# Kernel tuning notes

Measured on AMD Instinct MI355X. Metric: run time of the kernel, lower is better.

## Reference

```python
import jax, jax.numpy as jnp
import numpy as np

DEPTH = 30
IN_C, OUT_C, WIDTH = 1, 1, 1
DILATIONS = [i + 1 for i in range(10)]


def setup_inputs() -> dict:
    key = jax.random.key(0)
    ks = jax.random.split(key, 9)
    B, H, W = 4, 512, 512
    # MSDConvBlock weight init std from the source
    std = float(np.sqrt(2.0 / (9.0 * (IN_C + WIDTH * (DEPTH - 1)) + OUT_C)))
    x = jax.random.normal(ks[0], (B, IN_C, H, W), dtype=jnp.float32)
    # Wmsd[i, :i+1] are the 3x3 kernels at depth i: channel 0 acts on x,
    # channel z acts on hiddenstate z-1. Padded rows are unused.
    Wmsd = jax.random.normal(ks[1], (DEPTH, DEPTH, 3, 3), dtype=jnp.float32) * std
    bias = jax.random.normal(ks[2], (DEPTH,), dtype=jnp.float32) * 0.1  # shared per-depth bias
    # final 1x1 conv (zero-init in source; random here so the output is non-trivial)
    convW = jax.random.normal(ks[3], (OUT_C, WIDTH * DEPTH + IN_C, 1, 1), dtype=jnp.float32) * 0.1
    convB = jax.random.normal(ks[4], (OUT_C,), dtype=jnp.float32) * 0.1
    # ScalingBlocks: per-channel affine, identity init
    sin_w = jnp.ones((IN_C,), dtype=jnp.float32)
    sin_b = jnp.zeros((IN_C,), dtype=jnp.float32)
    sout_w = jnp.ones((OUT_C,), dtype=jnp.float32)
    sout_b = jnp.zeros((OUT_C,), dtype=jnp.float32)
    return {"x": x, "Wmsd": Wmsd, "bias": bias, "convW": convW, "convB": convB,
            "sin_w": sin_w, "sin_b": sin_b, "sout_w": sout_w, "sout_b": sout_b}


def _conv(x, w, dilation):
    # 'same' 3x3 dilated conv, NCHW / OIHW
    d = dilation
    return jax.lax.conv_general_dilated(
        x, w, window_strides=(1, 1), padding=[(d, d), (d, d)],
        rhs_dilation=(d, d), dimension_numbers=("NCHW", "OIHW", "NCHW"))


def reference(x, Wmsd, bias, convW, convB, sin_w, sin_b, sout_w, sout_b):
    depth = Wmsd.shape[0]
    x = x * sin_w[None, :, None, None] + sin_b[None, :, None, None]
    feats = x  # growing concat: [x, h0, h1, ...]
    for i in range(depth):
        d = DILATIONS[i % len(DILATIONS)]  # counter increments once per depth
        n_in = feats.shape[1]  # = IN_C + i (with width=1, IN_C=1)
        w = Wmsd[i, :n_in][None]  # [1, n_in, 3, 3]
        # sum of single-channel convs == one multi-channel conv over the concat
        h = _conv(feats, w, d)
        h = jax.nn.relu(h + bias[i])
        feats = jnp.concatenate([feats, h], axis=1)
    y = jax.lax.conv_general_dilated(
        feats, convW, window_strides=(1, 1), padding="VALID",
        dimension_numbers=("NCHW", "OIHW", "NCHW"))
    y = y + convB[None, :, None, None]
    y = y * sout_w[None, :, None, None] + sout_b[None, :, None, None]
    return y
```

## Files before the change

kernel.cpp:

```cpp
#include <hip/hip_runtime.h>


#define MSD_DEPTH 30
#define NB 4
#define IH 512
#define IW 512
#define HALO 16
#define WPp (IW + 2 * HALO)
#define HPp (IH + 2 * HALO)
#define PLANE_U ((size_t)WPp * HPp)
#define PSTR ((size_t)NB * PLANE_U)
#define NPAIR 15
#define NPIX (NB * IH * IW)
#define WPK_OFF ((size_t)20 << 20)
#define ZSTRIPS (32 * (WPp / 4) * NPAIR * NB)
#define SSTRIPS (512 * 8 * NPAIR * NB)
#define TOTZ (ZSTRIPS + SSTRIPS)

typedef _Float16 h2v __attribute__((ext_vector_type(2)));
typedef unsigned int u32;

__device__ __forceinline__ float fdot2u(u32 a, u32 b, float c) {
#if __has_builtin(__builtin_amdgcn_fdot2)
    return __builtin_amdgcn_fdot2(__builtin_bit_cast(h2v, a),
                                  __builtin_bit_cast(h2v, b), c, false);
#else
    h2v x = __builtin_bit_cast(h2v, a), y = __builtin_bit_cast(h2v, b);
    return c + (float)x[0] * (float)y[0] + (float)x[1] * (float)y[1];
#endif
}

__global__ __launch_bounds__(256) void preamble_kernel(const float* __restrict__ x,
                                                       const float* __restrict__ Wmsd,
                                                       const float* __restrict__ convW,
                                                       u32* __restrict__ feats,
                                                       u32* __restrict__ wpk,
                                                       u32* __restrict__ cpk,
                                                       const float* __restrict__ sw,
                                                       const float* __restrict__ sb) {
    int idx = blockIdx.x * 256 + threadIdx.x;

    if (idx < MSD_DEPTH * NPAIR * 9) {
        int I = idx / (NPAIR * 9);
        int rem = idx - I * (NPAIR * 9);
        int p = rem / 9, t = rem - p * 9;
        int NC = I + 1, c0 = 2 * p, c1 = 2 * p + 1;
        h2v pk;
        pk[0] = (_Float16)((c0 < NC) ? Wmsd[((size_t)I * MSD_DEPTH + c0) * 9 + t] : 0.f);
        pk[1] = (_Float16)((c1 < NC) ? Wmsd[((size_t)I * MSD_DEPTH + c1) * 9 + t] : 0.f);
        wpk[idx] = __builtin_bit_cast(u32, pk);
    }
    if (idx < NPAIR) {
        h2v pk;
        pk[0] = (_Float16)convW[2 * idx];
        pk[1] = (_Float16)convW[2 * idx + 1];
        cpk[idx] = __builtin_bit_cast(u32, pk);
    }

    if (idx < ZSTRIPS) {
        const int per = 32 * (WPp / 4);
        int sub = idx / per;
        int s = idx - sub * per;
        int rr = s / 136;
        int c4 = (s - rr * 136) * 4;
        int r = (rr < 16) ? rr : (IH + HALO) + (rr - 16);
        uint4 z = {0, 0, 0, 0};
        *(uint4*)(feats + (size_t)sub * PLANE_U + (size_t)r * WPp + c4) = z;
    } else if (idx < TOTZ) {
        int s = idx - ZSTRIPS;
        int sub = s >> 12;
        int rem = s & 4095;
        int r = HALO + (rem >> 3);
        int e = rem & 7;
        int c4 = (e < 4) ? (e * 4) : (IW + HALO + (e - 4) * 4);
        uint4 z = {0, 0, 0, 0};
        *(uint4*)(feats + (size_t)sub * PLANE_U + (size_t)r * WPp + c4) = z;
    }

    if (idx < NPIX / 8) {
        int pix = idx * 8;
        int b = pix >> 18;
        int y = (pix >> 9) & 511;
        int xx = pix & 511;
        const float sws = sw[0], sbs = sb[0];
        u32 v[8];
#pragma unroll
        for (int j = 0; j < 8; ++j) {
            _Float16 h = (_Float16)(x[pix + j] * sws + sbs);
            v[j] = (u32)__builtin_bit_cast(unsigned short, h);
        }
        u32* q = feats + (size_t)b * PLANE_U + (size_t)(y + HALO) * WPp + HALO + xx;
        *(uint4*)q = *(uint4*)&v[0];
        *(uint4*)(q + 4) = *(uint4*)&v[4];
    }
}

template <int I, int MINW>
__global__ __launch_bounds__(512, MINW) void depth_kernel(u32* __restrict__ feats,
                                                          const u32* __restrict__ wpk,
                                                          const u32* __restrict__ cpk,
                                                          const float* __restrict__ bias,
                                                          const float* __restrict__ convW,
                                                          const float* __restrict__ convB,
                                                          const float* __restrict__ soutw,
                                                          const float* __restrict__ soutb,
                                                          float* __restrict__ out) {
    constexpr int D = (I % 10) + 1;
    constexpr int NC = I + 1;
    constexpr int NP = (NC + 1) / 2;
    constexpr bool LAST = (I == MSD_DEPTH - 1);
    constexpr int C0 = (12 - D) >> 2;
    constexpr int C1 = (15 + D) >> 2;

    const int tid = threadIdx.x;
    const int widx = tid >> 6, lane = tid & 63;
    const int bid = blockIdx.x;
    const int xcd = bid & 7;
    const int kk = bid >> 3;
    const int b = xcd >> 1;
    const int y = (xcd & 1) * 256 + kk * 4 + (widx >> 1);
    const int h = widx & 1;
    const int xx = h * 256 + lane * 4;

    u32* const pb = feats + (size_t)b * PLANE_U + (size_t)(y + HALO) * WPp + HALO + xx;

    float acc[4], ydot[4];
#pragma unroll
    for (int j = 0; j < 4; ++j) { acc[j] = 0.f; ydot[j] = 0.f; }

    const u32* const wrb = wpk + (size_t)I * (NPAIR * 9);

    u32 A[3][28], B[3][28];

    auto load_pair = [&](u32 (*bp)[28], int p) {
        const u32* pp = pb + (size_t)p * PSTR;
#pragma unroll
        for (int r = 0; r < 3; ++r) {
            const u32* rp = pp + (ptrdiff_t)(r - 1) * (D * WPp);
#pragma unroll
            for (int c = C0; c <= C1; ++c)
                *(uint4*)&bp[r][4 * c] = *(const uint4*)(rp - 12 + 4 * c);
        }
    };

    auto compute = [&](u32 (*bp)[28], int p) {
        const u32* wq = wrb + p * 9;
        const u32 cw = LAST ? cpk[p] : 0u;
#pragma unroll
        for (int r = 0; r < 3; ++r) {
            const u32* s = bp[r];
            const u32 w0 = wq[r * 3 + 0], w1 = wq[r * 3 + 1], w2 = wq[r * 3 + 2];
#pragma unroll
            for (int k = 0; k < 4; ++k) {
                float a = acc[k];
                a = fdot2u(s[12 - D + k], w0, a);
                a = fdot2u(s[12 + k],     w1, a);
                a = fdot2u(s[12 + D + k], w2, a);
                acc[k] = a;
            }
            if (LAST && r == 1) {
#pragma unroll
                for (int k = 0; k < 4; ++k) ydot[k] = fdot2u(s[12 + k], cw, ydot[k]);
            }
        }
    };

    load_pair(A, 0);
    int p = 0;
    for (; p + 2 <= NP; p += 2) {
        load_pair(B, p + 1);
        compute(A, p);
        if (p + 2 < NP) load_pair(A, p + 2);
        compute(B, p + 1);
    }
    if (p < NP) compute(A, p);

    const float b0 = bias[I];
    if (!LAST) {
        u32 part[4];
        if constexpr ((NC & 1) != 0) {
            constexpr bool inA = (((NP - 1) & 1) == 0);
            const u32* s = inA ? A[1] : B[1];
#pragma unroll
            for (int j = 0; j < 4; ++j) part[j] = s[12 + j];
        }
        u32 mg[4];
#pragma unroll
        for (int j = 0; j < 4; ++j) {
            float hh = acc[j] + b0;
            hh = hh > 0.f ? hh : 0.f;
            u32 h16 = (u32)__builtin_bit_cast(unsigned short, (_Float16)hh);
            if constexpr ((NC & 1) != 0)
                mg[j] = (part[j] & 0xFFFFu) | (h16 << 16);
            else
                mg[j] = h16;
        }
        u32* q = feats + (size_t)(NC >> 1) * PSTR + (size_t)b * PLANE_U +
                 (size_t)(y + HALO) * WPp + HALO + xx;
        *(uint4*)q = *(uint4*)&mg[0];
    } else {
        const float cw30 = convW[MSD_DEPTH];
        const float cb = convB[0], ow = soutw[0], ob = soutb[0];
        float* q = out + ((size_t)b * IH + y) * IW + xx;
        float o[4];
#pragma unroll
        for (int j = 0; j < 4; ++j) {
            float hh = acc[j] + b0;
            hh = hh > 0.f ? hh : 0.f;
            float yv = ydot[j] + cw30 * hh + cb;
            o[j] = yv * ow + ob;
        }
        *(uint4*)q = *(uint4*)&o[0];
    }
}

extern "C" void kernel_launch(void* const* d_in, const int* in_sizes, int n_in,
                              void* d_out, int out_size, void* d_ws, size_t ws_size,
                              hipStream_t stream) {
    const float* x     = (const float*)d_in[0];
    const float* Wmsd  = (const float*)d_in[1];
    const float* bias  = (const float*)d_in[2];
    const float* convW = (const float*)d_in[3];
    const float* convB = (const float*)d_in[4];
    const float* sinw  = (const float*)d_in[5];
    const float* sinb  = (const float*)d_in[6];
    const float* soutw = (const float*)d_in[7];
    const float* soutb = (const float*)d_in[8];
    float* out = (float*)d_out;

    u32* feats = (u32*)d_ws;
    u32* wpk = feats + WPK_OFF;
    u32* cpk = wpk + MSD_DEPTH * NPAIR * 9;

    preamble_kernel<<<(TOTZ + 255) / 256, 256, 0, stream>>>(x, Wmsd, convW,
                                                            feats, wpk, cpk,
                                                            sinw, sinb);

#define LNCH(I)                                                                     \
    depth_kernel<I, (((I % 10) + 1 <= 4) ? 4 : 3)><<<512, 512, 0, stream>>>(        \
        feats, wpk, cpk, bias, convW, convB, soutw, soutb, out);
    LNCH(0)  LNCH(1)  LNCH(2)  LNCH(3)  LNCH(4)
    LNCH(5)  LNCH(6)  LNCH(7)  LNCH(8)  LNCH(9)
    LNCH(10) LNCH(11) LNCH(12) LNCH(13) LNCH(14)
    LNCH(15) LNCH(16) LNCH(17) LNCH(18) LNCH(19)
    LNCH(20) LNCH(21) LNCH(22) LNCH(23) LNCH(24)
    LNCH(25) LNCH(26) LNCH(27) LNCH(28) LNCH(29)
#undef LNCH
}
```

Baseline: 382.5 us.

## Fuse all depth layers into one cooperative kernel with per-row dataflow flags

After: 1.471 ms. +284.6%, slower.

```diff
diff --git a/kernel.cpp b/kernel.cpp
--- a/kernel.cpp
+++ b/kernel.cpp
@@ -12,6 +12,8 @@
 #define PSTR ((size_t)NB * PLANE_U)
 #define NPAIR 15
 #define NPIX (NB * IH * IW)
+#define FLAGS_OFF ((size_t)18 << 20)
+#define NFLAGS (MSD_DEPTH * NB * IH)
 #define WPK_OFF ((size_t)20 << 20)
 #define ZSTRIPS (32 * (WPp / 4) * NPAIR * NB)
 #define SSTRIPS (512 * 8 * NPAIR * NB)
@@ -28,6 +30,13 @@
     h2v x = __builtin_bit_cast(h2v, a), y = __builtin_bit_cast(h2v, b);
     return c + (float)x[0] * (float)y[0] + (float)x[1] * (float)y[1];
 #endif
+}
+
+__device__ __forceinline__ u32 aload_sys(const u32* p) {
+    return __hip_atomic_load(p, __ATOMIC_RELAXED, __HIP_MEMORY_SCOPE_SYSTEM);
+}
+__device__ __forceinline__ void astore_sys(u32* p, u32 v) {
+    __hip_atomic_store(p, v, __ATOMIC_RELAXED, __HIP_MEMORY_SCOPE_SYSTEM);
 }
 
 __global__ __launch_bounds__(256) void preamble_kernel(const float* __restrict__ x,
@@ -39,6 +48,8 @@
                                                        const float* __restrict__ sw,
                                                        const float* __restrict__ sb) {
     int idx = blockIdx.x * 256 + threadIdx.x;
+
+    if (idx < NFLAGS) feats[FLAGS_OFF + idx] = 0u;
 
     if (idx < MSD_DEPTH * NPAIR * 9) {
         int I = idx / (NPAIR * 9);
@@ -95,23 +106,181 @@
     }
 }
 
-template <int I, int MINW>
-__global__ __launch_bounds__(512, MINW) void depth_kernel(u32* __restrict__ feats,
-                                                          const u32* __restrict__ wpk,
-                                                          const u32* __restrict__ cpk,
-                                                          const float* __restrict__ bias,
-                                                          const float* __restrict__ convW,
-                                                          const float* __restrict__ convB,
-                                                          const float* __restrict__ soutw,
-                                                          const float* __restrict__ soutb,
-                                                          float* __restrict__ out) {
+template <int I, bool MEGA>
+__device__ __forceinline__ void depth_body(int b, int y, int xx, int lane,
+                                           u32* __restrict__ feats,
+                                           const u32* __restrict__ wpk,
+                                           const u32* __restrict__ cpk,
+                                           const float* __restrict__ bias,
+                                           const float* __restrict__ convW,
+                                           const float* __restrict__ convB,
+                                           const float* __restrict__ soutw,
+                                           const float* __restrict__ soutb,
+                                           float* __restrict__ out,
+                                           u32* __restrict__ flags) {
     constexpr int D = (I % 10) + 1;
     constexpr int NC = I + 1;
     constexpr int NP = (NC + 1) / 2;
     constexpr bool LAST = (I == MSD_DEPTH - 1);
     constexpr int C0 = (12 - D) >> 2;
     constexpr int C1 = (15 + D) >> 2;
-
+    constexpr bool HASAT = MEGA && (I >= 1);
+    constexpr int NPP = HASAT ? NP - 1 : NP;
+
+    if constexpr (HASAT) {
+        if (lane == 0) {
+            u32* fb = flags + ((size_t)(I - 1) * NB + b) * IH;
+#pragma unroll
+            for (int t = 0; t < 3; ++t) {
+                int r = (t == 0) ? (y - D) : (t == 1) ? y : (y + D);
+                if (r < 0 || r >= IH) continue;
+                while (__hip_atomic_load(&fb[r], __ATOMIC_RELAXED,
+                                         __HIP_MEMORY_SCOPE_SYSTEM) < 2u)
+                    __builtin_amdgcn_s_sleep(2);
+            }
+        }
+        asm volatile("" ::: "memory");
+        __builtin_amdgcn_sched_barrier(0);
+    }
+
+    u32* const pb = feats + (size_t)b * PLANE_U + (size_t)(y + HALO) * WPp + HALO + xx;
+
+    float acc[4], ydot[4];
+#pragma unroll
+    for (int j = 0; j < 4; ++j) { acc[j] = 0.f; ydot[j] = 0.f; }
+
+    const u32* const wrb = wpk + (size_t)I * (NPAIR * 9);
+
+    u32 A[3][28], B[3][28];
+
+    auto load_pair = [&](u32 (*bp)[28], int p) {
+        const u32* pp = pb + (size_t)p * PSTR;
+#pragma unroll
+        for (int r = 0; r < 3; ++r) {
+            const u32* rp = pp + (ptrdiff_t)(r - 1) * (D * WPp);
+#pragma unroll
+            for (int c = C0; c <= C1; ++c)
+                *(uint4*)&bp[r][4 * c] = *(const uint4*)(rp - 12 + 4 * c);
+        }
+    };
+
+    auto load_pair_at = [&](u32 (*bp)[28], int p) {
+        const u32* pp = pb + (size_t)p * PSTR;
+#pragma unroll
+        for (int r = 0; r < 3; ++r) {
+            const u32* rp = pp + (ptrdiff_t)(r - 1) * (D * WPp) - 12;
+#pragma unroll
+            for (int c = C0; c <= C1; ++c)
+#pragma unroll
+                for (int j = 0; j < 4; ++j)
+                    bp[r][4 * c + j] = aload_sys(rp + 4 * c + j);
+        }
+    };
+
+    auto compute = [&](u32 (*bp)[28], int p) {
+        const u32* wq = wrb + p * 9;
+        const u32 cw = LAST ? cpk[p] : 0u;
+#pragma unroll
+        for (int r = 0; r < 3; ++r) {
+            const u32* s = bp[r];
+            const u32 w0 = wq[r * 3 + 0], w1 = wq[r * 3 + 1], w2 = wq[r * 3 + 2];
+#pragma unroll
+            for (int k = 0; k < 4; ++k) {
+                float a = acc[k];
+                a = fdot2u(s[12 - D + k], w0, a);
+                a = fdot2u(s[12 + k],     w1, a);
+                a = fdot2u(s[12 + D + k], w2, a);
+                acc[k] = a;
+            }
+            if (LAST && r == 1) {
+#pragma unroll
+                for (int k = 0; k < 4; ++k) ydot[k] = fdot2u(s[12 + k], cw, ydot[k]);
+            }
+        }
+    };
+
+    if constexpr (NPP > 0) {
+        load_pair(A, 0);
+        int p = 0;
+        for (; p + 2 <= NPP; p += 2) {
+            load_pair(B, p + 1);
+            compute(A, p);
+            if (p + 2 < NPP) load_pair(A, p + 2);
+            compute(B, p + 1);
+        }
+        if (p < NPP) compute(A, p);
+    }
+
+    if constexpr (HASAT) {
+        load_pair_at(A, NP - 1);
+        compute(A, NP - 1);
+    }
+
+    const float b0 = bias[I];
+    if (!LAST) {
+        u32 part[4];
+        if constexpr ((NC & 1) != 0) {
+            if constexpr (HASAT) {
+#pragma unroll
+                for (int j = 0; j < 4; ++j) part[j] = A[1][12 + j];
+            } else {
+                constexpr bool inA = (((NP - 1) & 1) == 0);
+                const u32* s = inA ? A[1] : B[1];
+#pragma unroll
+                for (int j = 0; j < 4; ++j) part[j] = s[12 + j];
+            }
+        }
+        u32 mg[4];
+#pragma unroll
+        for (int j = 0; j < 4; ++j) {
+            float hh = acc[j] + b0;
+            hh = hh > 0.f ? hh : 0.f;
+            u32 h16 = (u32)__builtin_bit_cast(unsigned short, (_Float16)hh);
+            if constexpr ((NC & 1) != 0)
+                mg[j] = (part[j] & 0xFFFFu) | (h16 << 16);
+            else
+                mg[j] = h16;
+        }
+        u32* q = feats + (size_t)(NC >> 1) * PSTR + (size_t)b * PLANE_U +
+                 (size_t)(y + HALO) * WPp + HALO + xx;
+        if constexpr (MEGA) {
+            astore_sys(q + 0, mg[0]);
+            astore_sys(q + 1, mg[1]);
+            astore_sys(q + 2, mg[2]);
+            astore_sys(q + 3, mg[3]);
+            asm volatile("s_waitcnt vmcnt(0)" ::: "memory");
+            if (lane == 0)
+                __hip_atomic_fetch_add(flags + ((size_t)I * NB + b) * IH + y, 1u,
+                                       __ATOMIC_RELAXED, __HIP_MEMORY_SCOPE_SYSTEM);
+        } else {
+            *(uint4*)q = *(uint4*)&mg[0];
+        }
+    } else {
+        const float cw30 = convW[MSD_DEPTH];
+        const float cb = convB[0], ow = soutw[0], ob = soutb[0];
+        float* q = out + ((size_t)b * IH + y) * IW + xx;
+        float o[4];
+#pragma unroll
+        for (int j = 0; j < 4; ++j) {
+            float hh = acc[j] + b0;
+            hh = hh > 0.f ? hh : 0.f;
+            float yv = ydot[j] + cw30 * hh + cb;
+            o[j] = yv * ow + ob;
+        }
+        *(uint4*)q = *(uint4*)&o[0];
+    }
+}
+
+template <int I>
+__global__ __launch_bounds__(512, 4) void depth4_kernel(u32* __restrict__ feats,
+                                                        const u32* __restrict__ wpk,
+                                                        const u32* __restrict__ cpk,
+                                                        const float* __restrict__ bias,
+                                                        const float* __restrict__ convW,
+                                                        const float* __restrict__ convB,
+                                                        const float* __restrict__ soutw,
+                                                        const float* __restrict__ soutb,
+                                                        float* __restrict__ out) {
     const int tid = threadIdx.x;
     const int widx = tid >> 6, lane = tid & 63;
     const int bid = blockIdx.x;
@@ -121,97 +290,40 @@
     const int y = (xcd & 1) * 256 + kk * 4 + (widx >> 1);
     const int h = widx & 1;
     const int xx = h * 256 + lane * 4;
-
-    u32* const pb = feats + (size_t)b * PLANE_U + (size_t)(y + HALO) * WPp + HALO + xx;
-
-    float acc[4], ydot[4];
-#pragma unroll
-    for (int j = 0; j < 4; ++j) { acc[j] = 0.f; ydot[j] = 0.f; }
-
-    const u32* const wrb = wpk + (size_t)I * (NPAIR * 9);
-
-    u32 A[3][28], B[3][28];
-
-    auto load_pair = [&](u32 (*bp)[28], int p) {
-        const u32* pp = pb + (size_t)p * PSTR;
-#pragma unroll
-        for (int r = 0; r < 3; ++r) {
-            const u32* rp = pp + (ptrdiff_t)(r - 1) * (D * WPp);
-#pragma unroll
-            for (int c = C0; c <= C1; ++c)
-                *(uint4*)&bp[r][4 * c] = *(const uint4*)(rp - 12 + 4 * c);
-        }
-    };
-
-    auto compute = [&](u32 (*bp)[28], int p) {
-        const u32* wq = wrb + p * 9;
-        const u32 cw = LAST ? cpk[p] : 0u;
-#pragma unroll
-        for (int r = 0; r < 3; ++r) {
-            const u32* s = bp[r];
-            const u32 w0 = wq[r * 3 + 0], w1 = wq[r * 3 + 1], w2 = wq[r * 3 + 2];
-#pragma unroll
-            for (int k = 0; k < 4; ++k) {
-                float a = acc[k];
-                a = fdot2u(s[12 - D + k], w0, a);
-                a = fdot2u(s[12 + k],     w1, a);
-                a = fdot2u(s[12 + D + k], w2, a);
-                acc[k] = a;
-            }
-            if (LAST && r == 1) {
-#pragma unroll
-                for (int k = 0; k < 4; ++k) ydot[k] = fdot2u(s[12 + k], cw, ydot[k]);
-            }
-        }
-    };
-
-    load_pair(A, 0);
-    int p = 0;
-    for (; p + 2 <= NP; p += 2) {
-        load_pair(B, p + 1);
-        compute(A, p);
-        if (p + 2 < NP) load_pair(A, p + 2);
-        compute(B, p + 1);
-    }
-    if (p < NP) compute(A, p);
-
-    const float b0 = bias[I];
-    if (!LAST) {
-        u32 part[4];
-        if constexpr ((NC & 1) != 0) {
-            constexpr bool inA = (((NP - 1) & 1) == 0);
-            const u32* s = inA ? A[1] : B[1];
-#pragma unroll
-            for (int j = 0; j < 4; ++j) part[j] = s[12 + j];
-        }
-        u32 mg[4];
-#pragma unroll
-        for (int j = 0; j < 4; ++j) {
-            float hh = acc[j] + b0;
-            hh = hh > 0.f ? hh : 0.f;
-            u32 h16 = (u32)__builtin_bit_cast(unsigned short, (_Float16)hh);
-            if constexpr ((NC & 1) != 0)
-                mg[j] = (part[j] & 0xFFFFu) | (h16 << 16);
-            else
-                mg[j] = h16;
-        }
-        u32* q = feats + (size_t)(NC >> 1) * PSTR + (size_t)b * PLANE_U +
-                 (size_t)(y + HALO) * WPp + HALO + xx;
-        *(uint4*)q = *(uint4*)&mg[0];
-    } else {
-        const float cw30 = convW[MSD_DEPTH];
-        const float cb = convB[0], ow = soutw[0], ob = soutb[0];
-        float* q = out + ((size_t)b * IH + y) * IW + xx;
-        float o[4];
-#pragma unroll
-        for (int j = 0; j < 4; ++j) {
-            float hh = acc[j] + b0;
-            hh = hh > 0.f ? hh : 0.f;
-            float yv = ydot[j] + cw30 * hh + cb;
-            o[j] = yv * ow + ob;
-        }
-        *(uint4*)q = *(uint4*)&o[0];
-    }
+    depth_body<I, false>(b, y, xx, lane, feats, wpk, cpk, bias, convW, convB,
+                         soutw, soutb, out, nullptr);
+}
+
+__global__ __launch_bounds__(512, 4) void msd_mega(u32* __restrict__ feats,
+                                                   const u32* __restrict__ wpk,
+                                                   const u32* __restrict__ cpk,
+                                                   const float* __restrict__ bias,
+                                                   const float* __restrict__ convW,
+                                                   const float* __restrict__ convB,
+                                                   const float* __restrict__ soutw,
+                                                   const float* __restrict__ soutb,
+                                                   float* __restrict__ out,
+                                                   u32* __restrict__ flags) {
+    const int tid = threadIdx.x;
+    const int widx = tid >> 6, lane = tid & 63;
+    const int bid = blockIdx.x;
+    const int xcd = bid & 7;
+    const int kk = bid >> 3;
+    const int b = xcd >> 1;
+    const int y = (xcd & 1) * 256 + kk * 4 + (widx >> 1);
+    const int h = widx & 1;
+    const int xx = h * 256 + lane * 4;
+
+#define PH(I)                                                                  \
+    depth_body<I, true>(b, y, xx, lane, feats, wpk, cpk, bias, convW, convB,   \
+                        soutw, soutb, out, flags);
+    PH(0)  PH(1)  PH(2)  PH(3)  PH(4)
+    PH(5)  PH(6)  PH(7)  PH(8)  PH(9)
+    PH(10) PH(11) PH(12) PH(13) PH(14)
+    PH(15) PH(16) PH(17) PH(18) PH(19)
+    PH(20) PH(21) PH(22) PH(23) PH(24)
+    PH(25) PH(26) PH(27) PH(28) PH(29)
+#undef PH
 }
 
 extern "C" void kernel_launch(void* const* d_in, const int* in_sizes, int n_in,
@@ -229,6 +341,7 @@
     float* out = (float*)d_out;
 
     u32* feats = (u32*)d_ws;
+    u32* flags = feats + FLAGS_OFF;
     u32* wpk = feats + WPK_OFF;
     u32* cpk = wpk + MSD_DEPTH * NPAIR * 9;
 
@@ -236,14 +349,19 @@
                                                             feats, wpk, cpk,
                                                             sinw, sinb);
 
-#define LNCH(I)                                                                     \
-    depth_kernel<I, (((I % 10) + 1 <= 4) ? 4 : 3)><<<512, 512, 0, stream>>>(        \
-        feats, wpk, cpk, bias, convW, convB, soutw, soutb, out);
-    LNCH(0)  LNCH(1)  LNCH(2)  LNCH(3)  LNCH(4)
-    LNCH(5)  LNCH(6)  LNCH(7)  LNCH(8)  LNCH(9)
-    LNCH(10) LNCH(11) LNCH(12) LNCH(13) LNCH(14)
-    LNCH(15) LNCH(16) LNCH(17) LNCH(18) LNCH(19)
-    LNCH(20) LNCH(21) LNCH(22) LNCH(23) LNCH(24)
-    LNCH(25) LNCH(26) LNCH(27) LNCH(28) LNCH(29)
+    void* args[] = {&feats, &wpk, &cpk, &bias, &convW, &convB,
+                    &soutw, &soutb, &out, &flags};
+    hipError_t rc = hipLaunchCooperativeKernel(msd_mega, dim3(512), dim3(512),
+                                               args, 0u, stream);
+    if (rc != hipSuccess) {
+        (void)hipGetLastError();
+#define LNCH(I) depth4_kernel<I><<<512, 512, 0, stream>>>(feats, wpk, cpk, bias, convW, convB, soutw, soutb, out);
+        LNCH(0)  LNCH(1)  LNCH(2)  LNCH(3)  LNCH(4)
+        LNCH(5)  LNCH(6)  LNCH(7)  LNCH(8)  LNCH(9)
+        LNCH(10) LNCH(11) LNCH(12) LNCH(13) LNCH(14)
+        LNCH(15) LNCH(16) LNCH(17) LNCH(18) LNCH(19)
+        LNCH(20) LNCH(21) LNCH(22) LNCH(23) LNCH(24)
+        LNCH(25) LNCH(26) LNCH(27) LNCH(28) LNCH(29)
 #undef LNCH
-}
+    }
+}
```

## Fuse consecutive depth layers into one kernel with shared-memory halo recompute

Applied to the files above, without the earlier changes.

New measurement: 740.3 us. 1.94x slower.

```diff
diff --git a/kernel.cpp b/kernel.cpp
--- a/kernel.cpp
+++ b/kernel.cpp
@@ -95,122 +95,210 @@
     }
 }
 
-template <int I, int MINW>
-__global__ __launch_bounds__(512, MINW) void depth_kernel(u32* __restrict__ feats,
-                                                          const u32* __restrict__ wpk,
-                                                          const u32* __restrict__ cpk,
-                                                          const float* __restrict__ bias,
-                                                          const float* __restrict__ convW,
-                                                          const float* __restrict__ convB,
-                                                          const float* __restrict__ soutw,
-                                                          const float* __restrict__ soutb,
-                                                          float* __restrict__ out) {
-    constexpr int D = (I % 10) + 1;
-    constexpr int NC = I + 1;
-    constexpr int NP = (NC + 1) / 2;
-    constexpr bool LAST = (I == MSD_DEPTH - 1);
-    constexpr int C0 = (12 - D) >> 2;
-    constexpr int C1 = (15 + D) >> 2;
+template <int I>
+__global__ __launch_bounds__(512, 4) void fused_kernel(u32* __restrict__ feats,
+                                                       const u32* __restrict__ wpk,
+                                                       const u32* __restrict__ cpk,
+                                                       const float* __restrict__ bias,
+                                                       const float* __restrict__ convW,
+                                                       const float* __restrict__ convB,
+                                                       const float* __restrict__ soutw,
+                                                       const float* __restrict__ soutb,
+                                                       float* __restrict__ out) {
+    constexpr int D1 = (I % 10) + 1;
+    constexpr int D2 = ((I + 1) % 10) + 1;
+    constexpr int NP = I / 2 + 1;
+    constexpr bool LAST = (I == MSD_DEPTH - 2);
+    constexpr int HR = 4 + 2 * D2;
+    constexpr int ITER = HR / 4;
+    constexpr int C01 = (12 - D1) >> 2, C11 = (15 + D1) >> 2;
+    constexpr int C02 = (12 - D2) >> 2, C12 = (15 + D2) >> 2;
+    constexpr int LW = 544;
+
+    __shared__ u32 hl[HR][LW];
 
     const int tid = threadIdx.x;
-    const int widx = tid >> 6, lane = tid & 63;
+    const int w = tid >> 6, lane = tid & 63;
     const int bid = blockIdx.x;
     const int xcd = bid & 7;
     const int kk = bid >> 3;
     const int b = xcd >> 1;
-    const int y = (xcd & 1) * 256 + kk * 4 + (widx >> 1);
-    const int h = widx & 1;
-    const int xx = h * 256 + lane * 4;
-
-    u32* const pb = feats + (size_t)b * PLANE_U + (size_t)(y + HALO) * WPp + HALO + xx;
-
-    float acc[4], ydot[4];
-#pragma unroll
-    for (int j = 0; j < 4; ++j) { acc[j] = 0.f; ydot[j] = 0.f; }
-
-    const u32* const wrb = wpk + (size_t)I * (NPAIR * 9);
-
-    u32 A[3][28], B[3][28];
-
-    auto load_pair = [&](u32 (*bp)[28], int p) {
-        const u32* pp = pb + (size_t)p * PSTR;
-#pragma unroll
-        for (int r = 0; r < 3; ++r) {
-            const u32* rp = pp + (ptrdiff_t)(r - 1) * (D * WPp);
-#pragma unroll
-            for (int c = C0; c <= C1; ++c)
-                *(uint4*)&bp[r][4 * c] = *(const uint4*)(rp - 12 + 4 * c);
-        }
-    };
-
-    auto compute = [&](u32 (*bp)[28], int p) {
-        const u32* wq = wrb + p * 9;
-        const u32 cw = LAST ? cpk[p] : 0u;
-#pragma unroll
-        for (int r = 0; r < 3; ++r) {
-            const u32* s = bp[r];
-            const u32 w0 = wq[r * 3 + 0], w1 = wq[r * 3 + 1], w2 = wq[r * 3 + 2];
-#pragma unroll
-            for (int k = 0; k < 4; ++k) {
-                float a = acc[k];
-                a = fdot2u(s[12 - D + k], w0, a);
-                a = fdot2u(s[12 + k],     w1, a);
-                a = fdot2u(s[12 + D + k], w2, a);
-                acc[k] = a;
-            }
-            if (LAST && r == 1) {
-#pragma unroll
-                for (int k = 0; k < 4; ++k) ydot[k] = fdot2u(s[12 + k], cw, ydot[k]);
-            }
-        }
-    };
-
-    load_pair(A, 0);
-    int p = 0;
-    for (; p + 2 <= NP; p += 2) {
-        load_pair(B, p + 1);
-        compute(A, p);
-        if (p + 2 < NP) load_pair(A, p + 2);
-        compute(B, p + 1);
-    }
-    if (p < NP) compute(A, p);
-
-    const float b0 = bias[I];
-    if (!LAST) {
-        u32 part[4];
-        if constexpr ((NC & 1) != 0) {
+    const int y0 = (xcd & 1) * 256 + kk * 4;
+
+    const u32* const wrb1 = wpk + (size_t)I * (NPAIR * 9);
+    const float b1 = bias[I];
+
+    for (int t = 0; t < ITER; ++t) {
+        const int hh = w + 8 * t;
+        const int hrow = hh >> 1, half = hh & 1;
+        const int row = y0 - D2 + hrow;
+        const int xx = half * 256 + lane * 4;
+        if (lane < 16) hl[hrow][half ? (528 + lane) : lane] = 0u;
+        if (row < 0 || row >= IH) {
+#pragma unroll
+            for (int j = 0; j < 4; ++j) hl[hrow][16 + xx + j] = 0u;
+        } else {
+            u32* const pb = feats + (size_t)b * PLANE_U +
+                            (size_t)(row + HALO) * WPp + HALO + xx;
+            float acc[4];
+#pragma unroll
+            for (int j = 0; j < 4; ++j) acc[j] = 0.f;
+
+            u32 A[3][28], B[3][28];
+            auto load_pair = [&](u32 (*bp)[28], int p) {
+                const u32* pp = pb + (size_t)p * PSTR;
+#pragma unroll
+                for (int r = 0; r < 3; ++r) {
+                    const u32* rp = pp + (ptrdiff_t)(r - 1) * (D1 * WPp);
+#pragma unroll
+                    for (int c = C01; c <= C11; ++c)
+                        *(uint4*)&bp[r][4 * c] = *(const uint4*)(rp - 12 + 4 * c);
+                }
+            };
+            auto compute = [&](u32 (*bp)[28], int p) {
+                const u32* wq = wrb1 + p * 9;
+#pragma unroll
+                for (int r = 0; r < 3; ++r) {
+                    const u32* s = bp[r];
+                    const u32 w0 = wq[r * 3 + 0], w1 = wq[r * 3 + 1], w2 = wq[r * 3 + 2];
+#pragma unroll
+                    for (int k = 0; k < 4; ++k) {
+                        float a = acc[k];
+                        a = fdot2u(s[12 - D1 + k], w0, a);
+                        a = fdot2u(s[12 + k],      w1, a);
+                        a = fdot2u(s[12 + D1 + k], w2, a);
+                        acc[k] = a;
+                    }
+                }
+            };
+            load_pair(A, 0);
+            int p = 0;
+            for (; p + 2 <= NP; p += 2) {
+                load_pair(B, p + 1);
+                compute(A, p);
+                if (p + 2 < NP) load_pair(A, p + 2);
+                compute(B, p + 1);
+            }
+            if (p < NP) compute(A, p);
+
             constexpr bool inA = (((NP - 1) & 1) == 0);
-            const u32* s = inA ? A[1] : B[1];
-#pragma unroll
-            for (int j = 0; j < 4; ++j) part[j] = s[12 + j];
-        }
-        u32 mg[4];
-#pragma unroll
-        for (int j = 0; j < 4; ++j) {
-            float hh = acc[j] + b0;
-            hh = hh > 0.f ? hh : 0.f;
-            u32 h16 = (u32)__builtin_bit_cast(unsigned short, (_Float16)hh);
-            if constexpr ((NC & 1) != 0)
-                mg[j] = (part[j] & 0xFFFFu) | (h16 << 16);
-            else
-                mg[j] = h16;
-        }
-        u32* q = feats + (size_t)(NC >> 1) * PSTR + (size_t)b * PLANE_U +
-                 (size_t)(y + HALO) * WPp + HALO + xx;
-        *(uint4*)q = *(uint4*)&mg[0];
-    } else {
-        const float cw30 = convW[MSD_DEPTH];
-        const float cb = convB[0], ow = soutw[0], ob = soutb[0];
-        float* q = out + ((size_t)b * IH + y) * IW + xx;
-        float o[4];
-#pragma unroll
-        for (int j = 0; j < 4; ++j) {
-            float hh = acc[j] + b0;
-            hh = hh > 0.f ? hh : 0.f;
-            float yv = ydot[j] + cw30 * hh + cb;
-            o[j] = yv * ow + ob;
-        }
-        *(uint4*)q = *(uint4*)&o[0];
+            const u32* sc = inA ? A[1] : B[1];
+            u32 mg[4];
+#pragma unroll
+            for (int j = 0; j < 4; ++j) {
+                float hv = acc[j] + b1;
+                hv = hv > 0.f ? hv : 0.f;
+                u32 h16 = (u32)__builtin_bit_cast(unsigned short, (_Float16)hv);
+                mg[j] = (sc[12 + j] & 0xFFFFu) | (h16 << 16);
+            }
+#pragma unroll
+            for (int j = 0; j < 4; ++j) hl[hrow][16 + xx + j] = mg[j];
+            if constexpr (!LAST) {
+                if (row >= y0 && row < y0 + 4) {
+                    u32* q = feats + (size_t)(I / 2) * PSTR + (size_t)b * PLANE_U +
+                             (size_t)(row + HALO) * WPp + HALO + xx;
+                    *(uint4*)q = *(uint4*)&mg[0];
+                }
+            }
+        }
+    }
+    __syncthreads();
+
+    {
+        const int y = y0 + (w >> 1);
+        const int half = w & 1;
+        const int xx = half * 256 + lane * 4;
+        const u32* const wrb2 = wpk + (size_t)(I + 1) * (NPAIR * 9);
+        u32* const pb = feats + (size_t)b * PLANE_U +
+                        (size_t)(y + HALO) * WPp + HALO + xx;
+
+        float acc[4], ydot[4];
+#pragma unroll
+        for (int j = 0; j < 4; ++j) { acc[j] = 0.f; ydot[j] = 0.f; }
+
+        u32 A[3][28], B[3][28];
+        auto load_pair = [&](u32 (*bp)[28], int p) {
+            const u32* pp = pb + (size_t)p * PSTR;
+#pragma unroll
+            for (int r = 0; r < 3; ++r) {
+                const u32* rp = pp + (ptrdiff_t)(r - 1) * (D2 * WPp);
+#pragma unroll
+                for (int c = C02; c <= C12; ++c)
+                    *(uint4*)&bp[r][4 * c] = *(const uint4*)(rp - 12 + 4 * c);
+            }
+        };
+        auto compute = [&](u32 (*bp)[28], int p) {
+            const u32* wq = wrb2 + p * 9;
+            const u32 cw = LAST ? cpk[p] : 0u;
+#pragma unroll
+            for (int r = 0; r < 3; ++r) {
+                const u32* s = bp[r];
+                const u32 w0 = wq[r * 3 + 0], w1 = wq[r * 3 + 1], w2 = wq[r * 3 + 2];
+#pragma unroll
+                for (int k = 0; k < 4; ++k) {
+                    float a = acc[k];
+                    a = fdot2u(s[12 - D2 + k], w0, a);
+                    a = fdot2u(s[12 + k],      w1, a);
+                    a = fdot2u(s[12 + D2 + k], w2, a);
+                    acc[k] = a;
+                }
+                if (LAST && r == 1) {
+#pragma unroll
+                    for (int k = 0; k < 4; ++k) ydot[k] = fdot2u(s[12 + k], cw, ydot[k]);
+                }
+            }
+        };
+
+        if constexpr (NP > 1) {
+            load_pair(A, 0);
+            int p = 0;
+            for (; p + 2 <= NP - 1; p += 2) {
+                load_pair(B, p + 1);
+                compute(A, p);
+                if (p + 2 < NP - 1) load_pair(A, p + 2);
+                compute(B, p + 1);
+            }
+            if (p < NP - 1) compute(A, p);
+        }
+        {
+            const int lr0 = y - y0;
+            auto ldrow = [&](u32* dst, int lr) {
+#pragma unroll
+                for (int c = C02; c <= C12; ++c)
+                    *(uint4*)&dst[4 * c] = *(const uint4*)&hl[lr][16 + xx - 12 + 4 * c];
+            };
+            ldrow(A[0], lr0);
+            ldrow(A[1], lr0 + D2);
+            ldrow(A[2], lr0 + 2 * D2);
+            compute(A, NP - 1);
+        }
+
+        const float b2 = bias[I + 1];
+        if constexpr (!LAST) {
+            u32 mg[4];
+#pragma unroll
+            for (int j = 0; j < 4; ++j) {
+                float hv = acc[j] + b2;
+                hv = hv > 0.f ? hv : 0.f;
+                mg[j] = (u32)__builtin_bit_cast(unsigned short, (_Float16)hv);
+            }
+            u32* q = feats + (size_t)((I + 2) / 2) * PSTR + (size_t)b * PLANE_U +
+                     (size_t)(y + HALO) * WPp + HALO + xx;
+            *(uint4*)q = *(uint4*)&mg[0];
+        } else {
+            const float cw30 = convW[MSD_DEPTH];
+            const float cb = convB[0], ow = soutw[0], ob = soutb[0];
+            float* q = out + ((size_t)b * IH + y) * IW + xx;
+            float o[4];
+#pragma unroll
+            for (int j = 0; j < 4; ++j) {
+                float hv = acc[j] + b2;
+                hv = hv > 0.f ? hv : 0.f;
+                float yv = ydot[j] + cw30 * hv + cb;
+                o[j] = yv * ow + ob;
+            }
+            *(uint4*)q = *(uint4*)&o[0];
+        }
     }
 }
 
@@ -236,14 +324,9 @@
                                                             feats, wpk, cpk,
                                                             sinw, sinb);
 
-#define LNCH(I)                                                                     \
-    depth_kernel<I, (((I % 10) + 1 <= 4) ? 4 : 3)><<<512, 512, 0, stream>>>(        \
-        feats, wpk, cpk, bias, convW, convB, soutw, soutb, out);
-    LNCH(0)  LNCH(1)  LNCH(2)  LNCH(3)  LNCH(4)
-    LNCH(5)  LNCH(6)  LNCH(7)  LNCH(8)  LNCH(9)
-    LNCH(10) LNCH(11) LNCH(12) LNCH(13) LNCH(14)
-    LNCH(15) LNCH(16) LNCH(17) LNCH(18) LNCH(19)
-    LNCH(20) LNCH(21) LNCH(22) LNCH(23) LNCH(24)
-    LNCH(25) LNCH(26) LNCH(27) LNCH(28) LNCH(29)
+#define LNCH(I) fused_kernel<I><<<512, 512, 0, stream>>>(feats, wpk, cpk, bias, convW, convB, soutw, soutb, out);
+    LNCH(0)  LNCH(2)  LNCH(4)  LNCH(6)  LNCH(8)
+    LNCH(10) LNCH(12) LNCH(14) LNCH(16) LNCH(18)
+    LNCH(20) LNCH(22) LNCH(24) LNCH(26) LNCH(28)
 #undef LNCH
 }
```
